# Kernel optimization log

Measured on AMD Instinct MI355X. Metric: run time of the kernel, lower is better.

The kernel has to match this reference:

```python
import jax, jax.numpy as jnp
import numpy as np

CLIP = 10.0  # tanh clipping constant (Kool et al. C=10)


def setup_inputs() -> dict:
    key = jax.random.key(0)
    kq, kk, kv, km = jax.random.split(key, 4)
    B, M, N, D = 16, 2048, 2048, 128
    Q = jax.random.normal(kq, (B, M, D), dtype=jnp.float32)
    K = jax.random.normal(kk, (B, N, D), dtype=jnp.float32)
    V = jax.random.normal(kv, (B, N, D), dtype=jnp.float32)
    # mask: [B, N, 1] bool; True means "forbidden" (set logit to -inf).
    # p=0.3 so every row keeps plenty of valid keys (no all-masked rows).
    mask = jax.random.bernoulli(km, 0.3, (B, N, 1))
    return {"Q": Q, "K": K, "V": V, "mask": mask}


def reference(Q, K, V, mask):
    d_k = jnp.asarray(K.shape[-1], dtype=Q.dtype)
    # logits: [B, M, N]
    logits = jnp.einsum("bmd,bnd->bmn", Q, K) / jnp.sqrt(d_k)
    logits = CLIP * jnp.tanh(logits)
    # mask [B, N, 1] -> [B, 1, N], broadcast over query dim
    mask_t = jnp.transpose(mask, (0, 2, 1))
    logits = jnp.where(mask_t, -jnp.inf, logits)
    probs = jax.nn.softmax(logits, axis=-1)
    return jnp.einsum("bmn,bnd->bmd", probs, V)
```

## Files before the change

kernel.cpp:

```cpp
#include <hip/hip_runtime.h>
#include <hip/hip_fp16.h>

typedef _Float16 h8 __attribute__((ext_vector_type(8)));
typedef _Float16 h4 __attribute__((ext_vector_type(4)));
typedef float f32x4 __attribute__((ext_vector_type(4)));
typedef float f32x16 __attribute__((ext_vector_type(16)));

#define MFMA16(a, b, c) __builtin_amdgcn_mfma_f32_16x16x32_f16((a), (b), (c), 0, 0, 0)
#define MFMA32(a, b, c) __builtin_amdgcn_mfma_f32_32x32x16_f16((a), (b), (c), 0, 0, 0)

static constexpr int MM = 2048, NN = 2048, DD = 128;
static constexpr int MT = 64, KT = 64, NT = NN / KT;
static constexpr size_t KV_IMG = (size_t)16 * 32 * 16384;
static constexpr size_t WS_NEED = 2 * KV_IMG + 32768 * 4;

static constexpr float C1 = 0.25503487f;
static constexpr float C2 = 28.853900817779268f;
static constexpr float CVALID = 14.426950408889634f;
static constexpr float CMASK = -1.0e30f;

__device__ inline void glds16(const void* g, void* l) {
  __builtin_amdgcn_global_load_lds(
      (const __attribute__((address_space(1))) void*)g,
      (__attribute__((address_space(3))) void*)l, 16, 0, 0);
}

__global__ __launch_bounds__(256) void prep_bias(const void* __restrict__ mraw,
                                                 float* __restrict__ biasC) {
  const int tid = threadIdx.x;
  const unsigned int* mw = (const unsigned int*)mraw;
  const unsigned char* mb = (const unsigned char*)mraw;
  int okW = 1;
  for (int w = tid; w < 8192; w += 256) {
    unsigned int v = mw[w];
    okW &= (v == 0u || v == 1u || v == 0x3f800000u) ? 1 : 0;
  }
  __shared__ int sW;
  if (tid == 0) sW = 1;
  __syncthreads();
  if (!okW) atomicAnd(&sW, 0);
  __syncthreads();
  const int i = blockIdx.x * 256 + tid;
  bool masked = sW ? (mw[i] != 0u) : (mb[i] != 0);
  biasC[i] = masked ? CMASK : CVALID;
}

__global__ __launch_bounds__(256) void prep_all(
    const float* __restrict__ K, const float* __restrict__ V,
    const void* __restrict__ mraw, unsigned char* __restrict__ kimg,
    unsigned char* __restrict__ vimg, float* __restrict__ biasC) {
  const int id = blockIdx.x;
  const int tid = threadIdx.x;
  if (id >= 1024) {
    const unsigned int* mw = (const unsigned int*)mraw;
    const unsigned char* mb = (const unsigned char*)mraw;
    int okW = 1;
    for (int w = tid; w < 8192; w += 256) {
      unsigned int v = mw[w];
      okW &= (v == 0u || v == 1u || v == 0x3f800000u) ? 1 : 0;
    }
    __shared__ int sW;
    if (tid == 0) sW = 1;
    __syncthreads();
    if (!okW) atomicAnd(&sW, 0);
    __syncthreads();
    const int i = (id - 1024) * 256 + tid;
    bool masked = sW ? (mw[i] != 0u) : (mb[i] != 0);
    biasC[i] = masked ? CMASK : CVALID;
    return;
  }
  const int bt = id & 511;
  if (id < 512) {
    const float* src = K + (size_t)bt * KT * DD;
    unsigned char* dst = kimg + (size_t)bt * 16384;
#pragma unroll
    for (int it = 0; it < 4; ++it) {
      const int key = (tid >> 4) + 16 * it;
      const int o = tid & 15;
      f32x4 a = *(const f32x4*)(src + key * DD + 8 * o);
      f32x4 c = *(const f32x4*)(src + key * DD + 8 * o + 4);
      h8 hv;
#pragma unroll
      for (int j = 0; j < 4; ++j) {
        hv[j] = (_Float16)a[j];
        hv[j + 4] = (_Float16)c[j];
      }
      *(h8*)(dst + key * 256 + ((16 * o) ^ ((key & 7) << 4))) = hv;
    }
  } else {
    const float* src = V + (size_t)bt * KT * DD;
    unsigned char* dst = vimg + (size_t)bt * 16384;
    const int d = tid & 127;
    const int half = tid >> 7;
#pragma unroll
    for (int ki = 0; ki < 4; ++ki) {
      const int koct = half * 4 + ki;
      h8 w;
#pragma unroll
      for (int q = 0; q < 8; ++q)
        w[q] = (_Float16)src[(8 * koct + q) * DD + d];
      *(h8*)(dst + d * 128 + 16 * (koct ^ (d & 7))) = w;
    }
  }
}

__global__ __launch_bounds__(256, 2) void attn_main(
    const float* __restrict__ Qg, const unsigned char* __restrict__ kimg,
    const unsigned char* __restrict__ vimg, const float* __restrict__ biasC,
    float* __restrict__ out) {
  __shared__ __align__(16) unsigned char smem[76032];
  const int tid = threadIdx.x;
  const int lane = tid & 63;
  const int wv = tid >> 6;
  const int l31 = lane & 31;
  const int hp = lane >> 5;
  const int rw = wv >> 1;
  const int h = wv & 1;
  const int bid = blockIdx.x;
  const int swz = ((bid & 7) << 6) | (bid >> 3);
  const int b = swz >> 5;
  const int mt = swz & 31;
  const int m0 = mt * MT + rw * 32;

  h8 qa[8];
  {
    const float* qr = Qg + ((size_t)b * MM + m0 + l31) * DD;
#pragma unroll
    for (int st = 0; st < 8; ++st) {
      const int d0 = 16 * st + 8 * hp;
      f32x4 a = *(const f32x4*)(qr + d0);
      f32x4 c = *(const f32x4*)(qr + d0 + 4);
      h8 hi;
#pragma unroll
      for (int j = 0; j < 4; ++j) {
        hi[j] = (_Float16)a[j];
        hi[j + 4] = (_Float16)c[j];
      }
      qa[st] = hi;
    }
  }

  f32x16 oacc[4];
  f32x16 rsacc;
#pragma unroll
  for (int dc = 0; dc < 4; ++dc)
#pragma unroll
    for (int j = 0; j < 16; ++j) oacc[dc][j] = 0.f;
#pragma unroll
  for (int j = 0; j < 16; ++j) rsacc[j] = 0.f;

  h8 onesf;
#pragma unroll
  for (int j = 0; j < 8; ++j) onesf[j] = (_Float16)1.0f;

  const unsigned char* kib = kimg + (size_t)b * 32 * 16384;
  const unsigned char* vib = vimg + (size_t)b * 32 * 16384;
  const float* cb = biasC + b * NN;
  unsigned char* pscr = smem + 65536 + wv * 2560;

#pragma unroll
  for (int i = 0; i < 4; ++i) {
    const int off = wv * 4096 + i * 1024;
    glds16(kib + off + lane * 16, smem + off);
    glds16(vib + off + lane * 16, smem + 16384 + off);
  }
  __syncthreads();

  const int key = 32 * h + l31;
  const int krow = key << 8;
  const int ksw = (key & 7) << 4;

  for (int tn = 0; tn < NT; ++tn) {
    const unsigned char* kbuf = smem + (tn & 1) * 32768;
    const unsigned char* vbuf = kbuf + 16384;
    if (tn + 1 < NT) {
      unsigned char* nbuf = smem + ((tn + 1) & 1) * 32768;
      const unsigned char* ks = kib + (size_t)(tn + 1) * 16384;
      const unsigned char* vs = vib + (size_t)(tn + 1) * 16384;
#pragma unroll
      for (int i = 0; i < 4; ++i) {
        const int off = wv * 4096 + i * 1024;
        glds16(ks + off + lane * 16, nbuf + off);
        glds16(vs + off + lane * 16, nbuf + 16384 + off);
      }
    }

    const float Cc = cb[tn * KT + key];

    f32x16 s;
#pragma unroll
    for (int j = 0; j < 16; ++j) s[j] = 0.f;
    __builtin_amdgcn_s_setprio(1);
#pragma unroll
    for (int st = 0; st < 8; ++st) {
      h8 kf = *(const h8*)(kbuf + krow + ((32 * st + 16 * hp) ^ ksw));
      s = MFMA32(qa[st], kf, s);
    }
    __builtin_amdgcn_s_setprio(0);

#pragma unroll
    for (int j = 0; j < 16; ++j) {
      float u = __builtin_amdgcn_exp2f(s[j] * C1);
      float p = __builtin_amdgcn_exp2f(
          fmaf(-C2, __builtin_amdgcn_rcpf(u + 1.0f), Cc));
      const int qrow = (j & 3) + 8 * (j >> 2) + 4 * hp;
      *(_Float16*)(pscr + qrow * 80 + l31 * 2) = (_Float16)p;
    }
    h8 pa0 = *(const h8*)(pscr + l31 * 80 + 16 * hp);
    h8 pa1 = *(const h8*)(pscr + l31 * 80 + 32 + 16 * hp);
    __builtin_amdgcn_s_setprio(1);
    rsacc = MFMA32(pa0, onesf, rsacc);
    rsacc = MFMA32(pa1, onesf, rsacc);
#pragma unroll
    for (int dc = 0; dc < 4; ++dc) {
      const int d = 32 * dc + l31;
      const int vrow = d << 7;
      const int vsw = (d & 7) << 4;
      h8 vf0 = *(const h8*)(vbuf + vrow + ((64 * h + 16 * hp) ^ vsw));
      h8 vf1 = *(const h8*)(vbuf + vrow + ((64 * h + 32 + 16 * hp) ^ vsw));
      oacc[dc] = MFMA32(pa0, vf0, oacc[dc]);
      oacc[dc] = MFMA32(pa1, vf1, oacc[dc]);
    }
    __builtin_amdgcn_s_setprio(0);
    __syncthreads();
  }

  float* olds = (float*)smem;
  float* rslds = (float*)(smem + 75776);
  if (h == 1) {
#pragma unroll
    for (int j = 0; j < 16; ++j) {
      const int qrow = (j & 3) + 8 * (j >> 2) + 4 * hp;
#pragma unroll
      for (int dc = 0; dc < 4; ++dc)
        olds[(rw * 32 + qrow) * 128 + 32 * dc + l31] = oacc[dc][j];
      if (l31 == 0) rslds[rw * 32 + qrow] = rsacc[j];
    }
  }
  __syncthreads();
  if (h == 0) {
    float* ob = out + ((size_t)b * MM + m0) * DD;
#pragma unroll
    for (int j = 0; j < 16; ++j) {
      const int qrow = (j & 3) + 8 * (j >> 2) + 4 * hp;
      const float tot = rsacc[j] + rslds[rw * 32 + qrow];
      const float inv = __builtin_amdgcn_rcpf(tot);
#pragma unroll
      for (int dc = 0; dc < 4; ++dc) {
        float v = oacc[dc][j] + olds[(rw * 32 + qrow) * 128 + 32 * dc + l31];
        ob[qrow * DD + 32 * dc + l31] = v * inv;
      }
    }
  }
}

__global__ __launch_bounds__(256, 2) void attn_fallback(
    const float* __restrict__ Qg, const float* __restrict__ Kg,
    const float* __restrict__ Vg, const float* __restrict__ biasC,
    float* __restrict__ out) {
  __shared__ __align__(16) unsigned char smem[51456];
  const int tid = threadIdx.x;
  const int lane = tid & 63;
  const int wv = tid >> 6;
  const int r = lane & 15;
  const int g = lane >> 4;
  const int rw = wv >> 1;
  const int h = wv & 1;
  const int b = blockIdx.x >> 5;
  const int mt = blockIdx.x & 31;
  const int m0 = mt * MT + rw * 32;

  float* blds = (float*)(smem + 43264);
  {
    const float* cb = biasC + b * NN;
#pragma unroll
    for (int i = 0; i < 8; ++i) blds[tid + 256 * i] = cb[tid + 256 * i];
  }
  h8 qh[2][4];
  {
    const float* qb = Qg + ((size_t)b * MM + m0) * DD;
#pragma unroll
    for (int rf = 0; rf < 2; ++rf) {
      const float* qr = qb + (16 * rf + r) * DD;
#pragma unroll
      for (int t = 0; t < 4; ++t) {
        f32x4 a = *(const f32x4*)(qr + 32 * t + 8 * g);
        f32x4 c = *(const f32x4*)(qr + 32 * t + 8 * g + 4);
        h8 hi;
#pragma unroll
        for (int j = 0; j < 4; ++j) {
          hi[j] = (_Float16)a[j];
          hi[j + 4] = (_Float16)c[j];
        }
        qh[rf][t] = hi;
      }
    }
  }
  f32x4 acc[2][8];
#pragma unroll
  for (int rf = 0; rf < 2; ++rf)
#pragma unroll
    for (int cd = 0; cd < 8; ++cd) acc[rf][cd] = (f32x4){0.f, 0.f, 0.f, 0.f};
  float rs[2][4] = {{0.f, 0.f, 0.f, 0.f}, {0.f, 0.f, 0.f, 0.f}};
  const float* kb = Kg + (size_t)b * NN * DD;
  const float* vbp = Vg + (size_t)b * NN * DD;
  _Float16* plds = (_Float16*)(smem + 32768 + wv * 2560);
  const int bk0 = tid >> 5, bd0 = tid & 31;
  const int bk1 = (256 + tid) >> 5, bd1 = tid & 31;
  f32x4 kpre[8], vpre[8];
#pragma unroll
  for (int i = 0; i < 8; ++i) kpre[i] = *(const f32x4*)(kb + i * 1024 + tid * 4);
#pragma unroll
  for (int q = 0; q < 4; ++q) {
    vpre[q] = *(const f32x4*)(vbp + (4 * bk0 + q) * DD + 4 * bd0);
    vpre[4 + q] = *(const f32x4*)(vbp + (4 * bk1 + q) * DD + 4 * bd1);
  }
  for (int tn = 0; tn < NT; ++tn) {
#pragma unroll
    for (int i = 0; i < 8; ++i) {
      const int flat = i * 1024 + tid * 4;
      const int kkey = flat >> 7;
      const int d0 = flat & 127;
      h4 hv;
#pragma unroll
      for (int j = 0; j < 4; ++j) hv[j] = (_Float16)kpre[i][j];
      *(h4*)(smem + (kkey << 8) + ((d0 << 1) ^ ((kkey & 7) << 4))) = hv;
    }
#pragma unroll
    for (int it = 0; it < 2; ++it) {
      const int bk = it ? bk1 : bk0;
      const int bd = it ? bd1 : bd0;
#pragma unroll
      for (int p = 0; p < 4; ++p) {
        h4 w;
#pragma unroll
        for (int q = 0; q < 4; ++q) w[q] = (_Float16)vpre[it * 4 + q][p];
        const int d = 4 * bd + p;
        *(h4*)(smem + 16384 + (d << 7) +
               ((bk << 3) ^ (((d >> 1) & 7) << 4))) = w;
      }
    }
    if (tn + 1 < NT) {
      const float* ks = kb + (tn + 1) * KT * DD;
      const float* vs = vbp + (tn + 1) * KT * DD;
#pragma unroll
      for (int i = 0; i < 8; ++i) kpre[i] = *(const f32x4*)(ks + i * 1024 + tid * 4);
#pragma unroll
      for (int q = 0; q < 4; ++q) {
        vpre[q] = *(const f32x4*)(vs + (4 * bk0 + q) * DD + 4 * bd0);
        vpre[4 + q] = *(const f32x4*)(vs + (4 * bk1 + q) * DD + 4 * bd1);
      }
    }
    __syncthreads();
#pragma unroll
    for (int c = 0; c < 2; ++c) {
      f32x4 S0 = {0.f, 0.f, 0.f, 0.f}, S1 = {0.f, 0.f, 0.f, 0.f};
      const int kkey = h * 32 + 16 * c + r;
      const int krow = kkey << 8;
      const int ksw = (kkey & 7) << 4;
#pragma unroll
      for (int t = 0; t < 4; ++t) {
        h8 kf = *(const h8*)(smem + krow + ((64 * t + 16 * g) ^ ksw));
        S0 = MFMA16(qh[0][t], kf, S0);
        S1 = MFMA16(qh[1][t], kf, S1);
      }
      const float Cc = blds[tn * KT + kkey];
#pragma unroll
      for (int j = 0; j < 4; ++j) {
        float u0 = __builtin_amdgcn_exp2f(S0[j] * C1);
        float p0 = __builtin_amdgcn_exp2f(
            fmaf(-C2, __builtin_amdgcn_rcpf(u0 + 1.0f), Cc));
        rs[0][j] += p0;
        plds[(4 * g + j) * 40 + 16 * c + r] = (_Float16)p0;
        float u1 = __builtin_amdgcn_exp2f(S1[j] * C1);
        float p1 = __builtin_amdgcn_exp2f(
            fmaf(-C2, __builtin_amdgcn_rcpf(u1 + 1.0f), Cc));
        rs[1][j] += p1;
        plds[(16 + 4 * g + j) * 40 + 16 * c + r] = (_Float16)p1;
      }
    }
    h8 a0 = *(const h8*)((unsigned char*)plds + r * 80 + 16 * g);
    h8 a1 = *(const h8*)((unsigned char*)plds + (16 + r) * 80 + 16 * g);
#pragma unroll
    for (int cd = 0; cd < 8; ++cd) {
      const int d = 16 * cd + r;
      h8 vf = *(const h8*)(smem + 16384 + (d << 7) +
                           ((64 * h + 16 * g) ^ (((d >> 1) & 7) << 4)));
      acc[0][cd] = MFMA16(a0, vf, acc[0][cd]);
      acc[1][cd] = MFMA16(a1, vf, acc[1][cd]);
    }
    __syncthreads();
  }
#pragma unroll
  for (int rf = 0; rf < 2; ++rf)
#pragma unroll
    for (int j = 0; j < 4; ++j) {
      float v = rs[rf][j];
      v += __shfl_xor(v, 1);
      v += __shfl_xor(v, 2);
      v += __shfl_xor(v, 4);
      v += __shfl_xor(v, 8);
      rs[rf][j] = v;
    }
  float* olds = (float*)smem;
  float* rslds = (float*)(smem + 43008);
  if (h == 1) {
    float* my = olds + rw * 4096;
#pragma unroll
    for (int rf = 0; rf < 2; ++rf)
#pragma unroll
      for (int cd = 0; cd < 8; ++cd)
#pragma unroll
        for (int j = 0; j < 4; ++j)
          my[(16 * rf + 4 * g + j) * 128 + 16 * cd + r] = acc[rf][cd][j];
    if (r == 0) {
#pragma unroll
      for (int rf = 0; rf < 2; ++rf)
#pragma unroll
        for (int j = 0; j < 4; ++j)
          rslds[rw * 32 + 16 * rf + 4 * g + j] = rs[rf][j];
    }
  }
  __syncthreads();
  if (h == 0) {
    const float* ot = olds + rw * 4096;
    float* ob = out + ((size_t)b * MM + m0) * DD;
#pragma unroll
    for (int rf = 0; rf < 2; ++rf)
#pragma unroll
      for (int j = 0; j < 4; ++j) {
        const int rl = 16 * rf + 4 * g + j;
        const float tot = rs[rf][j] + rslds[rw * 32 + rl];
        const float inv = __builtin_amdgcn_rcpf(tot);
#pragma unroll
        for (int cd = 0; cd < 8; ++cd) {
          float v = acc[rf][cd][j] + ot[rl * 128 + 16 * cd + r];
          ob[rl * DD + 16 * cd + r] = v * inv;
        }
      }
  }
}

extern "C" void kernel_launch(void* const* d_in, const int* in_sizes, int n_in,
                              void* d_out, int out_size, void* d_ws, size_t ws_size,
                              hipStream_t stream) {
  const float* Q = (const float*)d_in[0];
  const float* K = (const float*)d_in[1];
  const float* V = (const float*)d_in[2];
  const void* mask = d_in[3];
  float* out = (float*)d_out;
  if (ws_size >= WS_NEED) {
    unsigned char* kimg = (unsigned char*)d_ws;
    unsigned char* vimg = kimg + KV_IMG;
    float* biasC = (float*)(kimg + 2 * KV_IMG);
    prep_all<<<dim3(1152), dim3(256), 0, stream>>>(K, V, mask, kimg, vimg, biasC);
    attn_main<<<dim3(512), dim3(256), 0, stream>>>(Q, kimg, vimg, biasC, out);
  } else {
    float* biasC = (float*)d_ws;
    prep_bias<<<dim3(128), dim3(256), 0, stream>>>(mask, biasC);
    attn_fallback<<<dim3(512), dim3(256), 0, stream>>>(Q, K, V, biasC, out);
  }
}
```

Measured before the change: 82.41 us.

## Use 128-row query tiles, bitmask masking, and register P transpose via permlane32_swap

The attention kernel now runs 512-thread blocks covering 128 query rows each, so each K/V tile staged in LDS is shared by twice as many waves and the grid halves. S is computed transposed (K times Q), which lets P be packed to fp16 and moved between lanes with permlane32_swap instead of going through an LDS scratch buffer. Row sums are now accumulated as scalars rather than with extra MFMAs against a ones vector. The mask is precomputed as 64-bit bitmasks instead of a float bias array. The epilogue stages output in padded LDS and writes it with coalesced vector stores. The trade-offs are higher register and LDS pressure per block and fewer blocks in flight.

```diff
diff --git a/kernel.cpp b/kernel.cpp
--- a/kernel.cpp
+++ b/kernel.cpp
@@ -5,14 +5,16 @@
 typedef _Float16 h4 __attribute__((ext_vector_type(4)));
 typedef float f32x4 __attribute__((ext_vector_type(4)));
 typedef float f32x16 __attribute__((ext_vector_type(16)));
+typedef unsigned int u32x2 __attribute__((ext_vector_type(2)));
+typedef unsigned int u32x4 __attribute__((ext_vector_type(4)));
 
 #define MFMA16(a, b, c) __builtin_amdgcn_mfma_f32_16x16x32_f16((a), (b), (c), 0, 0, 0)
 #define MFMA32(a, b, c) __builtin_amdgcn_mfma_f32_32x32x16_f16((a), (b), (c), 0, 0, 0)
 
 static constexpr int MM = 2048, NN = 2048, DD = 128;
-static constexpr int MT = 64, KT = 64, NT = NN / KT;
+static constexpr int KT = 64, NT = NN / KT;
 static constexpr size_t KV_IMG = (size_t)16 * 32 * 16384;
-static constexpr size_t WS_NEED = 2 * KV_IMG + 32768 * 4;
+static constexpr size_t WS_NEED = 2 * KV_IMG + 4096 + 32768 * 4;
 
 static constexpr float C1 = 0.25503487f;
 static constexpr float C2 = 28.853900817779268f;
@@ -29,7 +31,7 @@
                                                  float* __restrict__ biasC) {
   const int tid = threadIdx.x;
   const unsigned int* mw = (const unsigned int*)mraw;
-  const unsigned char* mb = (const unsigned char*)mraw;
+  const unsigned char* mby = (const unsigned char*)mraw;
   int okW = 1;
   for (int w = tid; w < 8192; w += 256) {
     unsigned int v = mw[w];
@@ -41,19 +43,19 @@
   if (!okW) atomicAnd(&sW, 0);
   __syncthreads();
   const int i = blockIdx.x * 256 + tid;
-  bool masked = sW ? (mw[i] != 0u) : (mb[i] != 0);
+  bool masked = sW ? (mw[i] != 0u) : (mby[i] != 0);
   biasC[i] = masked ? CMASK : CVALID;
 }
 
 __global__ __launch_bounds__(256) void prep_all(
     const float* __restrict__ K, const float* __restrict__ V,
     const void* __restrict__ mraw, unsigned char* __restrict__ kimg,
-    unsigned char* __restrict__ vimg, float* __restrict__ biasC) {
+    unsigned char* __restrict__ vimg, unsigned long long* __restrict__ m64) {
   const int id = blockIdx.x;
   const int tid = threadIdx.x;
   if (id >= 1024) {
     const unsigned int* mw = (const unsigned int*)mraw;
-    const unsigned char* mb = (const unsigned char*)mraw;
+    const unsigned char* mby = (const unsigned char*)mraw;
     int okW = 1;
     for (int w = tid; w < 8192; w += 256) {
       unsigned int v = mw[w];
@@ -64,9 +66,19 @@
     __syncthreads();
     if (!okW) atomicAnd(&sW, 0);
     __syncthreads();
-    const int i = (id - 1024) * 256 + tid;
-    bool masked = sW ? (mw[i] != 0u) : (mb[i] != 0);
-    biasC[i] = masked ? CMASK : CVALID;
+    const int p = (id - 1024) * 256 + tid;
+    const int base = p * 64;
+    unsigned long long bits = 0ull;
+    if (sW) {
+#pragma unroll 8
+      for (int k = 0; k < 64; ++k)
+        bits |= (unsigned long long)(mw[base + k] != 0u ? 1 : 0) << k;
+    } else {
+#pragma unroll 8
+      for (int k = 0; k < 64; ++k)
+        bits |= (unsigned long long)(mby[base + k] != 0 ? 1 : 0) << k;
+    }
+    m64[p] = bits;
     return;
   }
   const int bt = id & 511;
@@ -104,23 +116,22 @@
   }
 }
 
-__global__ __launch_bounds__(256, 2) void attn_main(
+__global__ __launch_bounds__(512, 2) void attn_main(
     const float* __restrict__ Qg, const unsigned char* __restrict__ kimg,
-    const unsigned char* __restrict__ vimg, const float* __restrict__ biasC,
-    float* __restrict__ out) {
-  __shared__ __align__(16) unsigned char smem[76032];
+    const unsigned char* __restrict__ vimg,
+    const unsigned long long* __restrict__ mask64, float* __restrict__ out) {
+  __shared__ __align__(16) unsigned char smem[68096];
   const int tid = threadIdx.x;
   const int lane = tid & 63;
   const int wv = tid >> 6;
   const int l31 = lane & 31;
   const int hp = lane >> 5;
-  const int rw = wv >> 1;
+  const int qg = wv >> 1;
   const int h = wv & 1;
   const int bid = blockIdx.x;
-  const int swz = ((bid & 7) << 6) | (bid >> 3);
-  const int b = swz >> 5;
-  const int mt = swz & 31;
-  const int m0 = mt * MT + rw * 32;
+  const int b = 2 * (bid & 7) + (bid >> 7);
+  const int mt = (bid >> 3) & 15;
+  const int m0 = mt * 128 + qg * 32;
 
   h8 qa[8];
   {
@@ -141,34 +152,28 @@
   }
 
   f32x16 oacc[4];
-  f32x16 rsacc;
 #pragma unroll
   for (int dc = 0; dc < 4; ++dc)
 #pragma unroll
     for (int j = 0; j < 16; ++j) oacc[dc][j] = 0.f;
-#pragma unroll
-  for (int j = 0; j < 16; ++j) rsacc[j] = 0.f;
-
-  h8 onesf;
-#pragma unroll
-  for (int j = 0; j < 8; ++j) onesf[j] = (_Float16)1.0f;
+  float rsl = 0.f;
 
   const unsigned char* kib = kimg + (size_t)b * 32 * 16384;
   const unsigned char* vib = vimg + (size_t)b * 32 * 16384;
-  const float* cb = biasC + b * NN;
-  unsigned char* pscr = smem + 65536 + wv * 2560;
-
-#pragma unroll
-  for (int i = 0; i < 4; ++i) {
-    const int off = wv * 4096 + i * 1024;
+  const unsigned long long* mtile = mask64 + (size_t)b * 32;
+
+#pragma unroll
+  for (int i = 0; i < 2; ++i) {
+    const int off = wv * 2048 + i * 1024;
     glds16(kib + off + lane * 16, smem + off);
     glds16(vib + off + lane * 16, smem + 16384 + off);
   }
   __syncthreads();
 
-  const int key = 32 * h + l31;
-  const int krow = key << 8;
-  const int ksw = (key & 7) << 4;
+  const int kr = 32 * h + l31;
+  const int krow = kr << 8;
+  const int ksw = (kr & 7) << 4;
+  const int baseSh = 32 * h + 4 * hp;
 
   for (int tn = 0; tn < NT; ++tn) {
     const unsigned char* kbuf = smem + (tn & 1) * 32768;
@@ -178,14 +183,13 @@
       const unsigned char* ks = kib + (size_t)(tn + 1) * 16384;
       const unsigned char* vs = vib + (size_t)(tn + 1) * 16384;
 #pragma unroll
-      for (int i = 0; i < 4; ++i) {
-        const int off = wv * 4096 + i * 1024;
+      for (int i = 0; i < 2; ++i) {
+        const int off = wv * 2048 + i * 1024;
         glds16(ks + off + lane * 16, nbuf + off);
         glds16(vs + off + lane * 16, nbuf + 16384 + off);
       }
     }
-
-    const float Cc = cb[tn * KT + key];
+    const unsigned long long mbits = mtile[tn];
 
     f32x16 s;
 #pragma unroll
@@ -194,23 +198,44 @@
 #pragma unroll
     for (int st = 0; st < 8; ++st) {
       h8 kf = *(const h8*)(kbuf + krow + ((32 * st + 16 * hp) ^ ksw));
-      s = MFMA32(qa[st], kf, s);
+      s = MFMA32(kf, qa[st], s);
     }
     __builtin_amdgcn_s_setprio(0);
 
-#pragma unroll
-    for (int j = 0; j < 16; ++j) {
-      float u = __builtin_amdgcn_exp2f(s[j] * C1);
-      float p = __builtin_amdgcn_exp2f(
-          fmaf(-C2, __builtin_amdgcn_rcpf(u + 1.0f), Cc));
-      const int qrow = (j & 3) + 8 * (j >> 2) + 4 * hp;
-      *(_Float16*)(pscr + qrow * 80 + l31 * 2) = (_Float16)p;
-    }
-    h8 pa0 = *(const h8*)(pscr + l31 * 80 + 16 * hp);
-    h8 pa1 = *(const h8*)(pscr + l31 * 80 + 32 + 16 * hp);
+    float p[16];
+#pragma unroll
+    for (int q = 0; q < 4; ++q) {
+      const unsigned nib = (unsigned)(mbits >> (baseSh + 8 * q)) & 0xFu;
+#pragma unroll
+      for (int i = 0; i < 4; ++i) {
+        const int rg = 4 * q + i;
+        const float Cc = ((nib >> i) & 1u) ? CMASK : CVALID;
+        const float u = __builtin_amdgcn_exp2f(s[rg] * C1);
+        const float pv = __builtin_amdgcn_exp2f(
+            fmaf(-C2, __builtin_amdgcn_rcpf(u + 1.0f), Cc));
+        p[rg] = pv;
+        rsl += pv;
+      }
+    }
+    unsigned pkA[4], pkB[4];
+#pragma unroll
+    for (int q = 0; q < 4; ++q) {
+      pkA[q] = __builtin_bit_cast(
+          unsigned, __builtin_amdgcn_cvt_pkrtz(p[4 * q + 0], p[4 * q + 1]));
+      pkB[q] = __builtin_bit_cast(
+          unsigned, __builtin_amdgcn_cvt_pkrtz(p[4 * q + 2], p[4 * q + 3]));
+    }
+    h8 pb[2];
+#pragma unroll
+    for (int ks = 0; ks < 2; ++ks) {
+      u32x2 sa = __builtin_amdgcn_permlane32_swap(pkA[2 * ks], pkA[2 * ks + 1],
+                                                  false, false);
+      u32x2 sb = __builtin_amdgcn_permlane32_swap(pkB[2 * ks], pkB[2 * ks + 1],
+                                                  false, false);
+      u32x4 w = {sa[0], sb[0], sa[1], sb[1]};
+      pb[ks] = __builtin_bit_cast(h8, w);
+    }
     __builtin_amdgcn_s_setprio(1);
-    rsacc = MFMA32(pa0, onesf, rsacc);
-    rsacc = MFMA32(pa1, onesf, rsacc);
 #pragma unroll
     for (int dc = 0; dc < 4; ++dc) {
       const int d = 32 * dc + l31;
@@ -218,39 +243,55 @@
       const int vsw = (d & 7) << 4;
       h8 vf0 = *(const h8*)(vbuf + vrow + ((64 * h + 16 * hp) ^ vsw));
       h8 vf1 = *(const h8*)(vbuf + vrow + ((64 * h + 32 + 16 * hp) ^ vsw));
-      oacc[dc] = MFMA32(pa0, vf0, oacc[dc]);
-      oacc[dc] = MFMA32(pa1, vf1, oacc[dc]);
+      oacc[dc] = MFMA32(vf0, pb[0], oacc[dc]);
+      oacc[dc] = MFMA32(vf1, pb[1], oacc[dc]);
     }
     __builtin_amdgcn_s_setprio(0);
     __syncthreads();
   }
 
+  u32x2 rr = __builtin_amdgcn_permlane32_swap(__float_as_uint(rsl),
+                                              __float_as_uint(rsl), false,
+                                              false);
+  const float totH = __uint_as_float(rr[0]) + __uint_as_float(rr[1]);
+
   float* olds = (float*)smem;
-  float* rslds = (float*)(smem + 75776);
+  float* rs1 = (float*)(smem + 67584);
+  const int row = qg * 32 + l31;
   if (h == 1) {
 #pragma unroll
-    for (int j = 0; j < 16; ++j) {
-      const int qrow = (j & 3) + 8 * (j >> 2) + 4 * hp;
-#pragma unroll
-      for (int dc = 0; dc < 4; ++dc)
-        olds[(rw * 32 + qrow) * 128 + 32 * dc + l31] = oacc[dc][j];
-      if (l31 == 0) rslds[rw * 32 + qrow] = rsacc[j];
-    }
+    for (int dc = 0; dc < 4; ++dc)
+#pragma unroll
+      for (int q = 0; q < 4; ++q) {
+        f32x4 v = {oacc[dc][4 * q + 0], oacc[dc][4 * q + 1],
+                   oacc[dc][4 * q + 2], oacc[dc][4 * q + 3]};
+        *(f32x4*)&olds[row * 132 + 32 * dc + 8 * q + 4 * hp] = v;
+      }
+    if (hp == 0) rs1[row] = totH;
   }
   __syncthreads();
   if (h == 0) {
-    float* ob = out + ((size_t)b * MM + m0) * DD;
-#pragma unroll
-    for (int j = 0; j < 16; ++j) {
-      const int qrow = (j & 3) + 8 * (j >> 2) + 4 * hp;
-      const float tot = rsacc[j] + rslds[rw * 32 + qrow];
-      const float inv = __builtin_amdgcn_rcpf(tot);
-#pragma unroll
-      for (int dc = 0; dc < 4; ++dc) {
-        float v = oacc[dc][j] + olds[(rw * 32 + qrow) * 128 + 32 * dc + l31];
-        ob[qrow * DD + 32 * dc + l31] = v * inv;
-      }
-    }
+    const float inv = __builtin_amdgcn_rcpf(totH + rs1[row]);
+#pragma unroll
+    for (int dc = 0; dc < 4; ++dc)
+#pragma unroll
+      for (int q = 0; q < 4; ++q) {
+        float* pp = &olds[row * 132 + 32 * dc + 8 * q + 4 * hp];
+        f32x4 v = *(const f32x4*)pp;
+        v[0] = (v[0] + oacc[dc][4 * q + 0]) * inv;
+        v[1] = (v[1] + oacc[dc][4 * q + 1]) * inv;
+        v[2] = (v[2] + oacc[dc][4 * q + 2]) * inv;
+        v[3] = (v[3] + oacc[dc][4 * q + 3]) * inv;
+        *(f32x4*)pp = v;
+      }
+  }
+  __syncthreads();
+  float* ob = out + ((size_t)b * MM + mt * 128) * DD;
+#pragma unroll
+  for (int c = 0; c < 8; ++c) {
+    const int idx = c * 2048 + tid * 4;
+    const int r2 = idx >> 7, col = idx & 127;
+    *(f32x4*)&ob[r2 * 128 + col] = *(const f32x4*)&olds[r2 * 132 + col];
   }
 }
 
@@ -268,7 +309,7 @@
   const int h = wv & 1;
   const int b = blockIdx.x >> 5;
   const int mt = blockIdx.x & 31;
-  const int m0 = mt * MT + rw * 32;
+  const int m0 = mt * 64 + rw * 32;
 
   float* blds = (float*)(smem + 43264);
   {
@@ -452,9 +493,9 @@
   if (ws_size >= WS_NEED) {
     unsigned char* kimg = (unsigned char*)d_ws;
     unsigned char* vimg = kimg + KV_IMG;
-    float* biasC = (float*)(kimg + 2 * KV_IMG);
-    prep_all<<<dim3(1152), dim3(256), 0, stream>>>(K, V, mask, kimg, vimg, biasC);
-    attn_main<<<dim3(512), dim3(256), 0, stream>>>(Q, kimg, vimg, biasC, out);
+    unsigned long long* m64 = (unsigned long long*)(vimg + KV_IMG);
+    prep_all<<<dim3(1026), dim3(256), 0, stream>>>(K, V, mask, kimg, vimg, m64);
+    attn_main<<<dim3(256), dim3(512), 0, stream>>>(Q, kimg, vimg, m64, out);
   } else {
     float* biasC = (float*)d_ws;
     prep_bias<<<dim3(128), dim3(256), 0, stream>>>(mask, biasC);
```

New measurement: 82.02 us. No clear change (-0.5%).
